# Kernel optimization log

Measured on AMD Instinct MI355X. Metric: run time of the kernel, lower is better.

## Reference

```python
import jax, jax.numpy as jnp
import numpy as np


def setup_inputs() -> dict:
    key = jax.random.key(0)
    k_x, k_q, k_k, k_v = jax.random.split(key, 4)
    B, S, D = 8, 1024, 768
    H, DH = 12, 64
    scale = 1.0 / np.sqrt(D)
    return {
        "x": jax.random.normal(k_x, (B, S, D), dtype=jnp.float32),
        "Wq": jax.random.normal(k_q, (H, D, DH), dtype=jnp.float32) * scale,
        "Wk": jax.random.normal(k_k, (H, D, DH), dtype=jnp.float32) * scale,
        "Wv": jax.random.normal(k_v, (H, D, DH), dtype=jnp.float32) * scale,
    }


def reference(x, Wq, Wk, Wv):
    # x: [B, S, D]; Wq/Wk/Wv: [H, D, DH] (per-head Linear weights, no bias)
    B, S, D = x.shape
    H, _, DH = Wq.shape
    q = jnp.einsum("bsd,hde->bhse", x, Wq)  # [B,H,S,DH]
    k = jnp.einsum("bsd,hde->bhse", x, Wk)
    v = jnp.einsum("bsd,hde->bhse", x, Wv)
    scores = jnp.einsum("bhse,bhte->bhst", q, k) / jnp.sqrt(jnp.float32(DH))
    causal = jnp.tril(jnp.ones((S, S), dtype=bool))  # keep lower triangle
    scores = jnp.where(causal, scores, -jnp.inf)
    attn = jax.nn.softmax(scores, axis=-1)  # dropout = 0.0 -> identity
    ctx = jnp.einsum("bhst,bhte->bhse", attn, v)  # [B,H,S,DH]
    # concat heads on last dim: [B,S,H*DH]
    return ctx.transpose(0, 2, 1, 3).reshape(B, S, H * DH)
```

## Files before the change

### kernel.cpp

```cpp
#include <hip/hip_runtime.h>


#define Bq 8
#define Sq 1024
#define Dq 768
#define Hq 12
#define DHq 64

typedef _Float16 f16;
typedef f16 f16x8 __attribute__((ext_vector_type(8)));
typedef float f32x4 __attribute__((ext_vector_type(4)));

#define MFMA16(a, b, c) __builtin_amdgcn_mfma_f32_16x16x32_f16(a, b, c, 0, 0, 0)

#define QSCL 0.1803368801111244f

#if __has_builtin(__builtin_amdgcn_exp2f)
#define EXP2(x) __builtin_amdgcn_exp2f(x)
#else
#define EXP2(x) exp2f(x)
#endif

__device__ __forceinline__ void gload16(const f16* g, f16* l) {
  __builtin_amdgcn_global_load_lds(
      (const __attribute__((address_space(1))) void*)g,
      (__attribute__((address_space(3))) void*)l, 16, 0, 0);
}

__global__ __launch_bounds__(256) void cvt_x_kernel(const float* __restrict__ x,
                                                    f16* __restrict__ xh) {
  int i = blockIdx.x * 256 + threadIdx.x;
  const float4* src = reinterpret_cast<const float4*>(x) + i * 2;
  float4 a = src[0], b = src[1];
  f16x8 o;
  o[0] = (f16)a.x; o[1] = (f16)a.y; o[2] = (f16)a.z; o[3] = (f16)a.w;
  o[4] = (f16)b.x; o[5] = (f16)b.y; o[6] = (f16)b.z; o[7] = (f16)b.w;
  *reinterpret_cast<f16x8*>(xh + i * 8) = o;
}

__global__ __launch_bounds__(256) void cvt_w_kernel(const float* __restrict__ Wq,
                                                    const float* __restrict__ Wk,
                                                    const float* __restrict__ Wv,
                                                    f16* __restrict__ WT) {
  __shared__ float tile[64][65];
  const int kt = blockIdx.x, h = blockIdx.y, w = blockIdx.z;
  const float* W = (w == 0) ? Wq : (w == 1) ? Wk : Wv;
  const int t = threadIdx.x;
  const int c0 = t & 63, r4 = t >> 6;
#pragma unroll
  for (int i = 0; i < 16; i++) {
    int kr = i * 4 + r4;
    tile[kr][c0] = W[((size_t)h * Dq + kt * 64 + kr) * DHq + c0];
  }
  __syncthreads();
#pragma unroll
  for (int i = 0; i < 16; i++) {
    int e2 = i * 4 + r4;
    WT[((size_t)(w * Hq + h) * DHq + e2) * Dq + kt * 64 + c0] = (f16)tile[c0][e2];
  }
}

__global__ __launch_bounds__(256) void proj_kernel(const f16* __restrict__ xh,
                                                   const f16* __restrict__ WT,
                                                   f16* __restrict__ Q,
                                                   f16* __restrict__ K,
                                                   f16* __restrict__ Vt) {
  __shared__ __align__(1024) f16 smem[30720];

  const int mt = blockIdx.x;
  const int h = blockIdx.y;
  const int row0 = mt * 128;
  const int t = threadIdx.x;
  const int wv = t >> 6;
  const int lane = t & 63;
  const int g = lane >> 4;
  const int ql = lane & 15;
  const int wvm = wv >> 1, wvn = wv & 1;

  const int lr = lane >> 2;
  const int scg = (lane & 3) ^ ((lane >> 3) & 3);

  const f16* xsrc = xh + (size_t)row0 * Dq;
  const f16* wsrc = WT + (size_t)h * DHq * Dq;

  const f16* gA0 = xsrc + (size_t)(wv * 32 + lr) * Dq + scg * 8;
  const f16* gA1 = gA0 + (size_t)16 * Dq;
  const int n0 = wv * 48 + lr, n1 = n0 + 16, n2 = n0 + 32;
  const f16* gB0 = wsrc + ((size_t)(n0 >> 6) * Hq * DHq + (n0 & 63)) * Dq + scg * 8;
  const f16* gB1 = wsrc + ((size_t)(n1 >> 6) * Hq * DHq + (n1 & 63)) * Dq + scg * 8;
  const f16* gB2 = wsrc + ((size_t)(n2 >> 6) * Hq * DHq + (n2 & 63)) * Dq + scg * 8;

  f32x4 acc[4][6] = {};

#define PROJ_STAGE(buf)                                              \
  do {                                                               \
    f16* sA_ = smem + (buf) * 4096 + wv * 1024;                      \
    f16* sB_ = smem + 12288 + (buf) * 6144 + wv * 1536;              \
    gload16(gA0, sA_); gload16(gA1, sA_ + 512);                      \
    gload16(gB0, sB_); gload16(gB1, sB_ + 512);                      \
    gload16(gB2, sB_ + 1024);                                        \
    gA0 += 32; gA1 += 32; gB0 += 32; gB1 += 32; gB2 += 32;           \
  } while (0)

  PROJ_STAGE(0);
  PROJ_STAGE(1);

  const int rq = (g ^ ((ql >> 1) & 3)) * 8;
  const f16* rA = smem + (wvm * 64 + ql) * 32 + rq;
  const f16* rB = smem + 12288 + (wvn * 96 + ql) * 32 + rq;

#pragma unroll
  for (int step = 0; step < 24; step++) {
    if (step < 23) asm volatile("s_waitcnt vmcnt(5) lgkmcnt(0)" ::: "memory");
    else           asm volatile("s_waitcnt vmcnt(0) lgkmcnt(0)" ::: "memory");
    __builtin_amdgcn_s_barrier();
    __builtin_amdgcn_sched_barrier(0);
    if (step < 22) PROJ_STAGE((step + 2) % 3);
    const int cur = step % 3;
    f16x8 af[4], bf[6];
#pragma unroll
    for (int mf = 0; mf < 4; mf++)
      af[mf] = *reinterpret_cast<const f16x8*>(rA + cur * 4096 + mf * 512);
#pragma unroll
    for (int nf = 0; nf < 6; nf++)
      bf[nf] = *reinterpret_cast<const f16x8*>(rB + cur * 6144 + nf * 512);
    __builtin_amdgcn_s_setprio(1);
#pragma unroll
    for (int mf = 0; mf < 4; mf++)
#pragma unroll
      for (int nf = 0; nf < 6; nf++)
        acc[mf][nf] = MFMA16(af[mf], bf[nf], acc[mf][nf]);
    __builtin_amdgcn_s_setprio(0);
  }
#undef PROJ_STAGE
  __syncthreads();

  const int b = row0 >> 10;
  const int s0 = row0 & 1023;
  const size_t base_sd = ((size_t)(b * Hq + h) * Sq) * DHq;

#pragma unroll
  for (int nf = 0; nf < 6; nf++) {
    const int c = wvn * 96 + nf * 16 + ql;
    const int w = c >> 6;
    if (w < 2) {
      f16* dst = (w == 0 ? Q : K);
      const float scl = (w == 0) ? QSCL : 1.0f;
      const int e = c & 63;
#pragma unroll
      for (int mf = 0; mf < 4; mf++) {
        const int sr = wvm * 64 + mf * 16 + g * 4;
#pragma unroll
        for (int r = 0; r < 4; r++)
          dst[base_sd + (size_t)(s0 + sr + r) * DHq + e] = (f16)(acc[mf][nf][r] * scl);
      }
    }
  }

  f16* vbuf = smem;
#pragma unroll
  for (int nf = 2; nf < 6; nf++) {
    if (wvn == 1) {
      const int e = (96 + nf * 16 + ql) & 63;
#pragma unroll
      for (int mf = 0; mf < 4; mf++) {
        const int sr = wvm * 64 + mf * 16 + g * 4;
        union { f16 hh[4]; uint2 u; } z;
#pragma unroll
        for (int r = 0; r < 4; r++) z.hh[r] = (f16)acc[mf][nf][r];
        *reinterpret_cast<uint2*>(&vbuf[e * 136 + sr]) = z.u;
      }
    }
  }
  __syncthreads();
#pragma unroll
  for (int i = 0; i < 4; i++) {
    int c = t + 256 * i;
    int e = c >> 4, p = (c & 15) * 8;
    *reinterpret_cast<uint4*>(Vt + base_sd + (size_t)e * Sq + s0 + p) =
        *reinterpret_cast<const uint4*>(vbuf + e * 136 + p);
  }
}

__global__ __launch_bounds__(256) void attn_kernel(const f16* __restrict__ Q,
                                                   const f16* __restrict__ K,
                                                   const f16* __restrict__ Vt,
                                                   float* __restrict__ out) {
  __shared__ __align__(16) f16 k_lds[2][64][72];
  __shared__ __align__(16) f16 vt_lds[2][64][72];

  const int L = blockIdx.x;
  const int i = L >> 3;
  const int bh = (L & 7) * Hq + (i % Hq);
  const int p = 7 - (i / Hq);
  const int MT = 2 * p + 1;
  const int t = threadIdx.x;
  const int wv = t >> 6;
  const int lane = t & 63;
  const int g = lane >> 4;
  const int ql = lane & 15;

  const f16* Qb = Q + (size_t)bh * Sq * DHq;
  const f16* Kb = K + (size_t)bh * Sq * DHq;
  const f16* Vtb = Vt + (size_t)bh * DHq * Sq;
  const int b = bh / Hq, h = bh % Hq;

  const int r0 = t >> 3;
  const int p0 = (t & 7) * 8;

  const int qg0 = 2 * p * 64 + wv * 16 + ql;
  const int qg1 = qg0 + 64;
  f16x8 qf[2][2];
  qf[0][0] = *reinterpret_cast<const f16x8*>(Qb + (size_t)qg0 * DHq + g * 8);
  qf[0][1] = *reinterpret_cast<const f16x8*>(Qb + (size_t)qg0 * DHq + 32 + g * 8);
  qf[1][0] = *reinterpret_cast<const f16x8*>(Qb + (size_t)qg1 * DHq + g * 8);
  qf[1][1] = *reinterpret_cast<const f16x8*>(Qb + (size_t)qg1 * DHq + 32 + g * 8);

  f32x4 o_acc[2][4] = {};
  float m_r[2] = { -__builtin_inff(), -__builtin_inff() };
  float l_r[2] = { 0.f, 0.f };

  uint4 kreg0, kreg1, vreg0, vreg1;
  kreg0 = *reinterpret_cast<const uint4*>(Kb + (size_t)r0 * DHq + p0);
  kreg1 = *reinterpret_cast<const uint4*>(Kb + (size_t)(32 + r0) * DHq + p0);
  vreg0 = *reinterpret_cast<const uint4*>(Vtb + (size_t)r0 * Sq + p0);
  vreg1 = *reinterpret_cast<const uint4*>(Vtb + (size_t)(32 + r0) * Sq + p0);
  *reinterpret_cast<uint4*>(&k_lds[0][r0][p0]) = kreg0;
  *reinterpret_cast<uint4*>(&k_lds[0][32 + r0][p0]) = kreg1;
  *reinterpret_cast<uint4*>(&vt_lds[0][r0][p0]) = vreg0;
  *reinterpret_cast<uint4*>(&vt_lds[0][32 + r0][p0]) = vreg1;
  kreg0 = *reinterpret_cast<const uint4*>(Kb + (size_t)(64 + r0) * DHq + p0);
  kreg1 = *reinterpret_cast<const uint4*>(Kb + (size_t)(96 + r0) * DHq + p0);
  vreg0 = *reinterpret_cast<const uint4*>(Vtb + (size_t)r0 * Sq + 64 + p0);
  vreg1 = *reinterpret_cast<const uint4*>(Vtb + (size_t)(32 + r0) * Sq + 64 + p0);
  __syncthreads();

  int cur = 0;
  for (int kt = 0; kt <= MT; kt++) {
    f16x8 kf[4][2], vf[4][2];
#pragma unroll
    for (int nt = 0; nt < 4; nt++) {
      kf[nt][0] = *reinterpret_cast<const f16x8*>(&k_lds[cur][nt * 16 + ql][g * 8]);
      kf[nt][1] = *reinterpret_cast<const f16x8*>(&k_lds[cur][nt * 16 + ql][32 + g * 8]);
      vf[nt][0] = *reinterpret_cast<const f16x8*>(&vt_lds[cur][nt * 16 + ql][g * 8]);
      vf[nt][1] = *reinterpret_cast<const f16x8*>(&vt_lds[cur][nt * 16 + ql][32 + g * 8]);
    }

#pragma unroll
    for (int qs = 0; qs < 2; qs++) {
      if (qs == 0 && kt > 2 * p) continue;
      f32x4 sf[4] = {};
      __builtin_amdgcn_s_setprio(1);
#pragma unroll
      for (int nt = 0; nt < 4; nt++) {
        sf[nt] = MFMA16(kf[nt][0], qf[qs][0], sf[nt]);
        sf[nt] = MFMA16(kf[nt][1], qf[qs][1], sf[nt]);
      }
      __builtin_amdgcn_s_setprio(0);

      if (kt == 2 * p + qs) {
#pragma unroll
        for (int nt = 0; nt < 4; nt++)
#pragma unroll
          for (int r = 0; r < 4; r++)
            if (nt * 16 + g * 4 + r > wv * 16 + ql) sf[nt][r] = -__builtin_inff();
      }

      float t0 = fmaxf(fmaxf(sf[0][0], sf[0][1]), fmaxf(sf[0][2], sf[0][3]));
      float t1 = fmaxf(fmaxf(sf[1][0], sf[1][1]), fmaxf(sf[1][2], sf[1][3]));
      float t2 = fmaxf(fmaxf(sf[2][0], sf[2][1]), fmaxf(sf[2][2], sf[2][3]));
      float t3 = fmaxf(fmaxf(sf[3][0], sf[3][1]), fmaxf(sf[3][2], sf[3][3]));
      float rowmax = fmaxf(fmaxf(t0, t1), fmaxf(t2, t3));
      rowmax = fmaxf(rowmax, __shfl_xor(rowmax, 16, 64));
      rowmax = fmaxf(rowmax, __shfl_xor(rowmax, 32, 64));

      if (!__all(rowmax <= m_r[qs] + 8.f)) {
        float mnew = fmaxf(m_r[qs], rowmax);
        float corr = EXP2(m_r[qs] - mnew);
        l_r[qs] *= corr;
#pragma unroll
        for (int nt = 0; nt < 4; nt++) {
          o_acc[qs][nt][0] *= corr; o_acc[qs][nt][1] *= corr;
          o_acc[qs][nt][2] *= corr; o_acc[qs][nt][3] *= corr;
        }
        m_r[qs] = mnew;
      }

      float pv[4][4];
#pragma unroll
      for (int nt = 0; nt < 4; nt++)
#pragma unroll
        for (int r = 0; r < 4; r++) pv[nt][r] = EXP2(sf[nt][r] - m_r[qs]);
      float s0 = (pv[0][0] + pv[0][1]) + (pv[0][2] + pv[0][3]);
      float s1 = (pv[1][0] + pv[1][1]) + (pv[1][2] + pv[1][3]);
      float s2 = (pv[2][0] + pv[2][1]) + (pv[2][2] + pv[2][3]);
      float s3 = (pv[3][0] + pv[3][1]) + (pv[3][2] + pv[3][3]);
      float rs = (s0 + s1) + (s2 + s3);
      rs += __shfl_xor(rs, 16, 64);
      rs += __shfl_xor(rs, 32, 64);
      l_r[qs] += rs;

      uint32_t pk[4][2];
#pragma unroll
      for (int nt = 0; nt < 4; nt++) {
        union { f16 hh[2]; uint32_t u; } z0, z1;
        z0.hh[0] = (f16)pv[nt][0]; z0.hh[1] = (f16)pv[nt][1];
        z1.hh[0] = (f16)pv[nt][2]; z1.hh[1] = (f16)pv[nt][3];
        pk[nt][0] = z0.u; pk[nt][1] = z1.u;
      }
      const int srcA = ((g & 1) * 2) * 16 + ql;
      const int srcB = srcA + 16;
      const bool selhi = (g >> 1) != 0;
      f16x8 pf[2];
#pragma unroll
      for (int ks = 0; ks < 2; ks++) {
        uint32_t aA0 = (uint32_t)__shfl((int)pk[2 * ks][0], srcA, 64);
        uint32_t aA1 = (uint32_t)__shfl((int)pk[2 * ks][1], srcA, 64);
        uint32_t aB0 = (uint32_t)__shfl((int)pk[2 * ks][0], srcB, 64);
        uint32_t aB1 = (uint32_t)__shfl((int)pk[2 * ks][1], srcB, 64);
        uint32_t bA0 = (uint32_t)__shfl((int)pk[2 * ks + 1][0], srcA, 64);
        uint32_t bA1 = (uint32_t)__shfl((int)pk[2 * ks + 1][1], srcA, 64);
        uint32_t bB0 = (uint32_t)__shfl((int)pk[2 * ks + 1][0], srcB, 64);
        uint32_t bB1 = (uint32_t)__shfl((int)pk[2 * ks + 1][1], srcB, 64);
        union { uint32_t w[4]; f16x8 v; } z;
        z.w[0] = selhi ? bA0 : aA0;
        z.w[1] = selhi ? bA1 : aA1;
        z.w[2] = selhi ? bB0 : aB0;
        z.w[3] = selhi ? bB1 : aB1;
        pf[ks] = z.v;
      }

      __builtin_amdgcn_s_setprio(1);
#pragma unroll
      for (int nt = 0; nt < 4; nt++) {
        o_acc[qs][nt] = MFMA16(vf[nt][0], pf[0], o_acc[qs][nt]);
        o_acc[qs][nt] = MFMA16(vf[nt][1], pf[1], o_acc[qs][nt]);
      }
      __builtin_amdgcn_s_setprio(0);
    }

    if (kt < MT) {
      *reinterpret_cast<uint4*>(&k_lds[cur ^ 1][r0][p0]) = kreg0;
      *reinterpret_cast<uint4*>(&k_lds[cur ^ 1][32 + r0][p0]) = kreg1;
      *reinterpret_cast<uint4*>(&vt_lds[cur ^ 1][r0][p0]) = vreg0;
      *reinterpret_cast<uint4*>(&vt_lds[cur ^ 1][32 + r0][p0]) = vreg1;
      if (kt + 2 <= MT) {
        const int kv0 = (kt + 2) * 64;
        kreg0 = *reinterpret_cast<const uint4*>(Kb + (size_t)(kv0 + r0) * DHq + p0);
        kreg1 = *reinterpret_cast<const uint4*>(Kb + (size_t)(kv0 + 32 + r0) * DHq + p0);
        vreg0 = *reinterpret_cast<const uint4*>(Vtb + (size_t)r0 * Sq + kv0 + p0);
        vreg1 = *reinterpret_cast<const uint4*>(Vtb + (size_t)(32 + r0) * Sq + kv0 + p0);
      }
    }
    __syncthreads();
    cur ^= 1;
  }

#pragma unroll
  for (int qs = 0; qs < 2; qs++) {
    const int qg = qs ? qg1 : qg0;
    float rl = 1.0f / l_r[qs];
    float* op = out + ((size_t)(b * Sq + qg)) * (Hq * DHq) + h * DHq;
#pragma unroll
    for (int nt = 0; nt < 4; nt++) {
      float4 st = { o_acc[qs][nt][0] * rl, o_acc[qs][nt][1] * rl,
                    o_acc[qs][nt][2] * rl, o_acc[qs][nt][3] * rl };
      *reinterpret_cast<float4*>(op + nt * 16 + g * 4) = st;
    }
  }
}

extern "C" void kernel_launch(void* const* d_in, const int* in_sizes, int n_in,
                              void* d_out, int out_size, void* d_ws, size_t ws_size,
                              hipStream_t stream) {
  const float* x = (const float*)d_in[0];
  const float* Wq = (const float*)d_in[1];
  const float* Wk = (const float*)d_in[2];
  const float* Wv = (const float*)d_in[3];
  float* out = (float*)d_out;

  const size_t off_xb = 0;
  const size_t off_wt = 12582912;
  const size_t off_q = 16121856;
  const size_t off_k = 28704768;
  const size_t off_v = 41287680;
  const size_t need = 53870592;
  if (ws_size < need) return;

  char* ws = (char*)d_ws;
  f16* xh = (f16*)(ws + off_xb);
  f16* WT = (f16*)(ws + off_wt);
  f16* Qd = (f16*)(ws + off_q);
  f16* Kd = (f16*)(ws + off_k);
  f16* Vtd = (f16*)(ws + off_v);

  cvt_x_kernel<<<3072, 256, 0, stream>>>(x, xh);
  cvt_w_kernel<<<dim3(12, 12, 3), 256, 0, stream>>>(Wq, Wk, Wv, WT);
  proj_kernel<<<dim3(64, 12), 256, 0, stream>>>(xh, WT, Qd, Kd, Vtd);
  attn_kernel<<<768, 256, 0, stream>>>(Qd, Kd, Vtd, out);
}
```

Measured before the change: 89.33 us.

## Stage P through per-wave LDS and issue next-tile stores before compute

```diff
diff --git a/kernel.cpp b/kernel.cpp
--- a/kernel.cpp
+++ b/kernel.cpp
@@ -188,6 +188,7 @@
                                                    float* __restrict__ out) {
   __shared__ __align__(16) f16 k_lds[2][64][72];
   __shared__ __align__(16) f16 vt_lds[2][64][72];
+  __shared__ __align__(16) f16 p_lds[4][16][72];
 
   const int L = blockIdx.x;
   const int i = L >> 3;
@@ -237,108 +238,6 @@
 
   int cur = 0;
   for (int kt = 0; kt <= MT; kt++) {
-    f16x8 kf[4][2], vf[4][2];
-#pragma unroll
-    for (int nt = 0; nt < 4; nt++) {
-      kf[nt][0] = *reinterpret_cast<const f16x8*>(&k_lds[cur][nt * 16 + ql][g * 8]);
-      kf[nt][1] = *reinterpret_cast<const f16x8*>(&k_lds[cur][nt * 16 + ql][32 + g * 8]);
-      vf[nt][0] = *reinterpret_cast<const f16x8*>(&vt_lds[cur][nt * 16 + ql][g * 8]);
-      vf[nt][1] = *reinterpret_cast<const f16x8*>(&vt_lds[cur][nt * 16 + ql][32 + g * 8]);
-    }
-
-#pragma unroll
-    for (int qs = 0; qs < 2; qs++) {
-      if (qs == 0 && kt > 2 * p) continue;
-      f32x4 sf[4] = {};
-      __builtin_amdgcn_s_setprio(1);
-#pragma unroll
-      for (int nt = 0; nt < 4; nt++) {
-        sf[nt] = MFMA16(kf[nt][0], qf[qs][0], sf[nt]);
-        sf[nt] = MFMA16(kf[nt][1], qf[qs][1], sf[nt]);
-      }
-      __builtin_amdgcn_s_setprio(0);
-
-      if (kt == 2 * p + qs) {
-#pragma unroll
-        for (int nt = 0; nt < 4; nt++)
-#pragma unroll
-          for (int r = 0; r < 4; r++)
-            if (nt * 16 + g * 4 + r > wv * 16 + ql) sf[nt][r] = -__builtin_inff();
-      }
-
-      float t0 = fmaxf(fmaxf(sf[0][0], sf[0][1]), fmaxf(sf[0][2], sf[0][3]));
-      float t1 = fmaxf(fmaxf(sf[1][0], sf[1][1]), fmaxf(sf[1][2], sf[1][3]));
-      float t2 = fmaxf(fmaxf(sf[2][0], sf[2][1]), fmaxf(sf[2][2], sf[2][3]));
-      float t3 = fmaxf(fmaxf(sf[3][0], sf[3][1]), fmaxf(sf[3][2], sf[3][3]));
-      float rowmax = fmaxf(fmaxf(t0, t1), fmaxf(t2, t3));
-      rowmax = fmaxf(rowmax, __shfl_xor(rowmax, 16, 64));
-      rowmax = fmaxf(rowmax, __shfl_xor(rowmax, 32, 64));
-
-      if (!__all(rowmax <= m_r[qs] + 8.f)) {
-        float mnew = fmaxf(m_r[qs], rowmax);
-        float corr = EXP2(m_r[qs] - mnew);
-        l_r[qs] *= corr;
-#pragma unroll
-        for (int nt = 0; nt < 4; nt++) {
-          o_acc[qs][nt][0] *= corr; o_acc[qs][nt][1] *= corr;
-          o_acc[qs][nt][2] *= corr; o_acc[qs][nt][3] *= corr;
-        }
-        m_r[qs] = mnew;
-      }
-
-      float pv[4][4];
-#pragma unroll
-      for (int nt = 0; nt < 4; nt++)
-#pragma unroll
-        for (int r = 0; r < 4; r++) pv[nt][r] = EXP2(sf[nt][r] - m_r[qs]);
-      float s0 = (pv[0][0] + pv[0][1]) + (pv[0][2] + pv[0][3]);
-      float s1 = (pv[1][0] + pv[1][1]) + (pv[1][2] + pv[1][3]);
-      float s2 = (pv[2][0] + pv[2][1]) + (pv[2][2] + pv[2][3]);
-      float s3 = (pv[3][0] + pv[3][1]) + (pv[3][2] + pv[3][3]);
-      float rs = (s0 + s1) + (s2 + s3);
-      rs += __shfl_xor(rs, 16, 64);
-      rs += __shfl_xor(rs, 32, 64);
-      l_r[qs] += rs;
-
-      uint32_t pk[4][2];
-#pragma unroll
-      for (int nt = 0; nt < 4; nt++) {
-        union { f16 hh[2]; uint32_t u; } z0, z1;
-        z0.hh[0] = (f16)pv[nt][0]; z0.hh[1] = (f16)pv[nt][1];
-        z1.hh[0] = (f16)pv[nt][2]; z1.hh[1] = (f16)pv[nt][3];
-        pk[nt][0] = z0.u; pk[nt][1] = z1.u;
-      }
-      const int srcA = ((g & 1) * 2) * 16 + ql;
-      const int srcB = srcA + 16;
-      const bool selhi = (g >> 1) != 0;
-      f16x8 pf[2];
-#pragma unroll
-      for (int ks = 0; ks < 2; ks++) {
-        uint32_t aA0 = (uint32_t)__shfl((int)pk[2 * ks][0], srcA, 64);
-        uint32_t aA1 = (uint32_t)__shfl((int)pk[2 * ks][1], srcA, 64);
-        uint32_t aB0 = (uint32_t)__shfl((int)pk[2 * ks][0], srcB, 64);
-        uint32_t aB1 = (uint32_t)__shfl((int)pk[2 * ks][1], srcB, 64);
-        uint32_t bA0 = (uint32_t)__shfl((int)pk[2 * ks + 1][0], srcA, 64);
-        uint32_t bA1 = (uint32_t)__shfl((int)pk[2 * ks + 1][1], srcA, 64);
-        uint32_t bB0 = (uint32_t)__shfl((int)pk[2 * ks + 1][0], srcB, 64);
-        uint32_t bB1 = (uint32_t)__shfl((int)pk[2 * ks + 1][1], srcB, 64);
-        union { uint32_t w[4]; f16x8 v; } z;
-        z.w[0] = selhi ? bA0 : aA0;
-        z.w[1] = selhi ? bA1 : aA1;
-        z.w[2] = selhi ? bB0 : aB0;
-        z.w[3] = selhi ? bB1 : aB1;
-        pf[ks] = z.v;
-      }
-
-      __builtin_amdgcn_s_setprio(1);
-#pragma unroll
-      for (int nt = 0; nt < 4; nt++) {
-        o_acc[qs][nt] = MFMA16(vf[nt][0], pf[0], o_acc[qs][nt]);
-        o_acc[qs][nt] = MFMA16(vf[nt][1], pf[1], o_acc[qs][nt]);
-      }
-      __builtin_amdgcn_s_setprio(0);
-    }
-
     if (kt < MT) {
       *reinterpret_cast<uint4*>(&k_lds[cur ^ 1][r0][p0]) = kreg0;
       *reinterpret_cast<uint4*>(&k_lds[cur ^ 1][32 + r0][p0]) = kreg1;
@@ -352,6 +251,90 @@
         vreg1 = *reinterpret_cast<const uint4*>(Vtb + (size_t)(32 + r0) * Sq + kv0 + p0);
       }
     }
+
+    f16x8 kf[4][2], vf[4][2];
+#pragma unroll
+    for (int nt = 0; nt < 4; nt++) {
+      kf[nt][0] = *reinterpret_cast<const f16x8*>(&k_lds[cur][nt * 16 + ql][g * 8]);
+      kf[nt][1] = *reinterpret_cast<const f16x8*>(&k_lds[cur][nt * 16 + ql][32 + g * 8]);
+      vf[nt][0] = *reinterpret_cast<const f16x8*>(&vt_lds[cur][nt * 16 + ql][g * 8]);
+      vf[nt][1] = *reinterpret_cast<const f16x8*>(&vt_lds[cur][nt * 16 + ql][32 + g * 8]);
+    }
+
+#pragma unroll
+    for (int qs = 0; qs < 2; qs++) {
+      if (qs == 0 && kt > 2 * p) continue;
+      f32x4 sf[4] = {};
+      __builtin_amdgcn_s_setprio(1);
+#pragma unroll
+      for (int nt = 0; nt < 4; nt++) {
+        sf[nt] = MFMA16(kf[nt][0], qf[qs][0], sf[nt]);
+        sf[nt] = MFMA16(kf[nt][1], qf[qs][1], sf[nt]);
+      }
+      __builtin_amdgcn_s_setprio(0);
+
+      if (kt == 2 * p + qs) {
+#pragma unroll
+        for (int nt = 0; nt < 4; nt++)
+#pragma unroll
+          for (int r = 0; r < 4; r++)
+            if (nt * 16 + g * 4 + r > wv * 16 + ql) sf[nt][r] = -__builtin_inff();
+      }
+
+      float t0 = fmaxf(fmaxf(sf[0][0], sf[0][1]), fmaxf(sf[0][2], sf[0][3]));
+      float t1 = fmaxf(fmaxf(sf[1][0], sf[1][1]), fmaxf(sf[1][2], sf[1][3]));
+      float t2 = fmaxf(fmaxf(sf[2][0], sf[2][1]), fmaxf(sf[2][2], sf[2][3]));
+      float t3 = fmaxf(fmaxf(sf[3][0], sf[3][1]), fmaxf(sf[3][2], sf[3][3]));
+      float rowmax = fmaxf(fmaxf(t0, t1), fmaxf(t2, t3));
+      rowmax = fmaxf(rowmax, __shfl_xor(rowmax, 16, 64));
+      rowmax = fmaxf(rowmax, __shfl_xor(rowmax, 32, 64));
+
+      if (!__all(rowmax <= m_r[qs] + 8.f)) {
+        float mnew = fmaxf(m_r[qs], rowmax);
+        float corr = EXP2(m_r[qs] - mnew);
+        l_r[qs] *= corr;
+#pragma unroll
+        for (int nt = 0; nt < 4; nt++) {
+          o_acc[qs][nt][0] *= corr; o_acc[qs][nt][1] *= corr;
+          o_acc[qs][nt][2] *= corr; o_acc[qs][nt][3] *= corr;
+        }
+        m_r[qs] = mnew;
+      }
+
+      float pv[4][4];
+#pragma unroll
+      for (int nt = 0; nt < 4; nt++)
+#pragma unroll
+        for (int r = 0; r < 4; r++) pv[nt][r] = EXP2(sf[nt][r] - m_r[qs]);
+      float s0 = (pv[0][0] + pv[0][1]) + (pv[0][2] + pv[0][3]);
+      float s1 = (pv[1][0] + pv[1][1]) + (pv[1][2] + pv[1][3]);
+      float s2 = (pv[2][0] + pv[2][1]) + (pv[2][2] + pv[2][3]);
+      float s3 = (pv[3][0] + pv[3][1]) + (pv[3][2] + pv[3][3]);
+      float rs = (s0 + s1) + (s2 + s3);
+      rs += __shfl_xor(rs, 16, 64);
+      rs += __shfl_xor(rs, 32, 64);
+      l_r[qs] += rs;
+
+#pragma unroll
+      for (int nt = 0; nt < 4; nt++) {
+        union { f16 hh[4]; uint2 u; } z;
+        z.hh[0] = (f16)pv[nt][0]; z.hh[1] = (f16)pv[nt][1];
+        z.hh[2] = (f16)pv[nt][2]; z.hh[3] = (f16)pv[nt][3];
+        *reinterpret_cast<uint2*>(&p_lds[wv][ql][nt * 16 + g * 4]) = z.u;
+      }
+      f16x8 pf[2];
+      pf[0] = *reinterpret_cast<const f16x8*>(&p_lds[wv][ql][g * 8]);
+      pf[1] = *reinterpret_cast<const f16x8*>(&p_lds[wv][ql][32 + g * 8]);
+
+      __builtin_amdgcn_s_setprio(1);
+#pragma unroll
+      for (int nt = 0; nt < 4; nt++) {
+        o_acc[qs][nt] = MFMA16(vf[nt][0], pf[0], o_acc[qs][nt]);
+        o_acc[qs][nt] = MFMA16(vf[nt][1], pf[1], o_acc[qs][nt]);
+      }
+      __builtin_amdgcn_s_setprio(0);
+    }
+
     __syncthreads();
     cur ^= 1;
   }
```

Result: faster. 84.05 us (-5.9%).
